# Optimization experiments

Measured on AMD Instinct MI355X. Metric: run time of the kernel, lower is better.

## Reference

```python
import jax, jax.numpy as jnp
import numpy as np

B, T = 128, 512
V, E, U, K = 50000, 100, 128, 32


def _lstm(x, Wk, Wr, b):
    # x: [B, T, D] -> [B, T, U], Keras LSTM gate order i,f,g,o
    Bd = x.shape[0]
    Ud = Wr.shape[0]
    xs = jnp.swapaxes(x, 0, 1)  # [T, B, D]

    def step(carry, xt):
        h, c = carry
        z = xt @ Wk + h @ Wr + b
        i, f, g, o = jnp.split(z, 4, axis=-1)
        c = jax.nn.sigmoid(f) * c + jax.nn.sigmoid(i) * jnp.tanh(g)
        h = jax.nn.sigmoid(o) * jnp.tanh(c)
        return (h, c), h

    init = (jnp.zeros((Bd, Ud), x.dtype), jnp.zeros((Bd, Ud), x.dtype))
    _, hs = jax.lax.scan(step, init, xs)
    return jnp.swapaxes(hs, 0, 1)


def _crf_logZ(em, trans):
    # em: [B, T, K] emissions; trans: [K, K]. Forward algorithm log-partition.
    alpha0 = em[:, 0]  # [B, K]
    es = jnp.swapaxes(em[:, 1:], 0, 1)  # [T-1, B, K]

    def step(alpha, et):
        # alpha[b, i] + trans[i, j] -> logsumexp over i, plus emission
        alpha = jax.nn.logsumexp(alpha[:, :, None] + trans[None], axis=1) + et
        return alpha, None

    alphaT, _ = jax.lax.scan(step, alpha0, es)
    return jax.nn.logsumexp(alphaT, axis=-1)  # [B]


def setup_inputs() -> dict:
    key = jax.random.key(0)
    ks = jax.random.split(key, 11)
    s = 0.1
    return {
        "tokens": jax.random.randint(ks[0], (B, T), 0, V, dtype=jnp.int32),
        "emb": jax.random.normal(ks[1], (V, E), jnp.float32) * s,
        "Wk_f": jax.random.normal(ks[2], (E, 4 * U), jnp.float32) * s,
        "Wr_f": jax.random.normal(ks[3], (U, 4 * U), jnp.float32) * s,
        "b_f": jnp.zeros((4 * U,), jnp.float32),
        "Wk_b": jax.random.normal(ks[4], (E, 4 * U), jnp.float32) * s,
        "Wr_b": jax.random.normal(ks[5], (U, 4 * U), jnp.float32) * s,
        "b_b": jnp.zeros((4 * U,), jnp.float32),
        "crf_kernel": jax.random.normal(ks[6], (2 * U, K), jnp.float32) * s,
        "crf_bias": jnp.zeros((K,), jnp.float32),
        "trans": jax.random.normal(ks[7], (K, K), jnp.float32) * s,
    }


def reference(tokens, emb, Wk_f, Wr_f, b_f, Wk_b, Wr_b, b_b, crf_kernel, crf_bias, trans):
    x = emb[tokens]  # [B, T, E]
    h_f = _lstm(x, Wk_f, Wr_f, b_f)
    h_b = _lstm(x[:, ::-1], Wk_b, Wr_b, b_b)[:, ::-1]
    h = jnp.concatenate([h_f, h_b], axis=-1)  # [B, T, 2U] (dropout = identity at inference)
    em = h @ crf_kernel + crf_bias  # [B, T, K] CRF emission potentials
    return _crf_logZ(em, trans)  # [B] log-partition via CRF forward DP
```

## Files before the change

kernel.cpp:

```cpp
#include <hip/hip_runtime.h>
#include <hip/hip_bf16.h>

#define B_  128
#define T_  512
#define V_  50000
#define VP  50016
#define E_  100
#define U_  128
#define K_  32
#define G4  512
#define KP  128
#define GRP 8

typedef _Float16 h2_t __attribute__((ext_vector_type(2)));
typedef _Float16 f16x8 __attribute__((ext_vector_type(8)));
typedef __fp16   h2raw_t __attribute__((ext_vector_type(2)));
typedef short    bf16x8 __attribute__((ext_vector_type(8)));
typedef float    f32x4  __attribute__((ext_vector_type(4)));

__device__ __forceinline__ h2_t pk2(float a, float b) {
    h2raw_t r = __builtin_amdgcn_cvt_pkrtz(a, b);
    union { h2raw_t r; h2_t h; } u; u.r = r; return u.h;
}
__device__ __forceinline__ int h2_as_int(h2_t v) { union { h2_t h; int i; } u; u.h = v; return u.i; }

#if __has_builtin(__builtin_amdgcn_rcpf)
__device__ __forceinline__ float rcp_f(float x) { return __builtin_amdgcn_rcpf(x); }
#else
__device__ __forceinline__ float rcp_f(float x) { return 1.f / x; }
#endif

__device__ __forceinline__ unsigned short bf16_bits(float v) {
    __hip_bfloat16 b = __float2bfloat16(v);
    union { __hip_bfloat16 b; unsigned short s; } u; u.b = b; return u.s;
}

__global__ __launch_bounds__(128) void pack_b_kernel(
    const float* __restrict__ Wk_f, const float* __restrict__ Wk_b,
    __hip_bfloat16* __restrict__ Bb)
{
    const int n = blockIdx.x;
    const int k = threadIdx.x;
    float v = 0.f;
    if (k < E_) v = (n < 512) ? Wk_f[k * 512 + n] : Wk_b[k * 512 + (n - 512)];
    Bb[n * KP + k] = __float2bfloat16(v);
}

__global__ __launch_bounds__(256, 2) void proj_mfma_kernel(
    const float* __restrict__ emb,
    const __hip_bfloat16* __restrict__ Bb,
    const float* __restrict__ b_f, const float* __restrict__ b_b,
    __hip_bfloat16* __restrict__ proj)
{
    const int r0   = blockIdx.x * 32;
    const int tid  = threadIdx.x;
    const int wv   = tid >> 6;
    const int lane = tid & 63;
    const int quad = lane >> 4;
    const int l16  = lane & 15;

    __shared__ __align__(16) float C_lds[32][268];
    unsigned short* A_st = (unsigned short*)&C_lds[0][0];

    for (int idx = tid; idx < 32 * 64; idx += 256) {
        int r = idx >> 6, kk = idx & 63;
        int vr = r0 + r; if (vr >= V_) vr = V_ - 1;
        unsigned int w = 0;
        if (kk < 50) {
            float2 v = *(const float2*)(emb + (long long)vr * E_ + 2 * kk);
            w = ((unsigned int)bf16_bits(v.y) << 16) | bf16_bits(v.x);
        }
        *(unsigned int*)&A_st[r * 136 + 2 * kk] = w;
    }
    __syncthreads();

    bf16x8 af[2][4];
    #pragma unroll
    for (int mt = 0; mt < 2; ++mt)
        #pragma unroll
        for (int kc = 0; kc < 4; ++kc)
            af[mt][kc] = *(const bf16x8*)&A_st[(mt * 16 + l16) * 136 +
                                               kc * 32 + quad * 8];
    __syncthreads();

    const unsigned short* Bu = (const unsigned short*)Bb;

    for (int ng = 0; ng < 4; ++ng) {
        const int n0 = ng * 256;

        bf16x8 bfr[4][4];
        #pragma unroll
        for (int nt = 0; nt < 4; ++nt)
            #pragma unroll
            for (int kc = 0; kc < 4; ++kc)
                bfr[nt][kc] = *(const bf16x8*)(Bu +
                    (n0 + wv * 64 + nt * 16 + l16) * KP + kc * 32 + quad * 8);

        f32x4 acc[2][4];
        #pragma unroll
        for (int mt = 0; mt < 2; ++mt)
            #pragma unroll
            for (int nt = 0; nt < 4; ++nt)
                acc[mt][nt] = (f32x4){0.f, 0.f, 0.f, 0.f};

        #pragma unroll
        for (int mt = 0; mt < 2; ++mt)
            #pragma unroll
            for (int nt = 0; nt < 4; ++nt)
                #pragma unroll
                for (int kc = 0; kc < 4; ++kc)
                    acc[mt][nt] = __builtin_amdgcn_mfma_f32_16x16x32_bf16(
                        af[mt][kc], bfr[nt][kc], acc[mt][nt], 0, 0, 0);

        #pragma unroll
        for (int mt = 0; mt < 2; ++mt)
            #pragma unroll
            for (int nt = 0; nt < 4; ++nt)
                #pragma unroll
                for (int v = 0; v < 4; ++v)
                    C_lds[mt * 16 + quad * 4 + v][wv * 64 + nt * 16 + l16] =
                        acc[mt][nt][v];
        __syncthreads();

        const float* bias = (n0 < 512) ? b_f : b_b;
        const int nbase = n0 & 511;
        for (int idx = tid; idx < 32 * 128; idx += 256) {
            int r = idx >> 7, cc = (idx & 127) * 2;
            float v0 = C_lds[r][cc]     + bias[nbase + cc];
            float v1 = C_lds[r][cc + 1] + bias[nbase + cc + 1];
            unsigned int w = ((unsigned int)bf16_bits(v1) << 16) | bf16_bits(v0);
            *(unsigned int*)(proj + (long long)(r0 + r) * 1024 + n0 + cc) = w;
        }
        __syncthreads();
    }
}

__device__ __forceinline__ float sigmoid_f(float x) {
    return rcp_f(1.f + __expf(-x));
}
__device__ __forceinline__ float tanh_f(float x) {
    return 1.f - 2.f * rcp_f(__expf(2.f * x) + 1.f);
}

__global__ __launch_bounds__(512, 1) void lstm_kernel(
    const __hip_bfloat16* __restrict__ proj,
    const int* __restrict__ tokens,
    const float* __restrict__ Wr_f, const float* __restrict__ Wr_b,
    __hip_bfloat16* __restrict__ h_buf)
{
    const int bid  = blockIdx.x;
    const int dir  = bid >> 7;
    const int b    = bid & 127;
    const int tid  = threadIdx.x;
    const int w    = tid >> 6;
    const int lane = tid & 63;
    const int quad = lane >> 4;
    const int l16  = lane & 15;

    const float* Wr = dir ? Wr_b : Wr_f;

    union uf16 { f16x8 v; h2_t p[4]; uint4 u; };
    f16x8 wb[4][4];
    #pragma unroll
    for (int tt = 0; tt < 4; ++tt) {
        const int col = 64 * w + 16 * tt + l16;
        #pragma unroll
        for (int kc = 0; kc < 4; ++kc) {
            const int k0 = kc * 32 + quad * 8;
            uf16 u;
            #pragma unroll
            for (int jj = 0; jj < 4; ++jj)
                u.p[jj] = pk2(Wr[(k0 + 2 * jj)     * G4 + col],
                              Wr[(k0 + 2 * jj + 1) * G4 + col]);
            wb[tt][kc] = u.v;
        }
    }

    __shared__ __align__(16) unsigned int hpl[64];
    __shared__ float zl[G4];
    if (tid < 64) hpl[tid] = 0;
    float c = 0.f;
    __syncthreads();

    const int tbase = b * T_;
    const long long rowbase = (long long)b * T_;
    const __hip_bfloat16* pr = proj + dir * 512 + tid;

    int tok_cur[GRP], tok_nxt[GRP];
    #pragma unroll
    for (int d = 0; d < GRP; ++d) {
        int t0 = dir ? (T_ - 1 - d) : d;
        tok_cur[d] = tokens[tbase + t0];
        int t1 = dir ? (T_ - 1 - (GRP + d)) : (GRP + d);
        tok_nxt[d] = tokens[tbase + t1];
    }

    float xk_cur[GRP][4];
    #pragma unroll
    for (int d = 0; d < GRP; ++d)
        #pragma unroll
        for (int g = 0; g < 4; ++g)
            xk_cur[d][g] = (tid < U_)
                ? __bfloat162float(pr[(long long)tok_cur[d] * 1024 + g * 128])
                : 0.f;

    unsigned int hpack[GRP];
    #pragma unroll
    for (int d = 0; d < GRP; ++d) hpack[d] = 0;

    for (int g = 0; g < T_ / GRP; ++g) {
        float xk_nxt[GRP][4];
        #pragma unroll
        for (int d = 0; d < GRP; ++d)
            #pragma unroll
            for (int gg = 0; gg < 4; ++gg) xk_nxt[d][gg] = 0.f;
        if (tid < U_ && g + 1 < T_ / GRP) {
            #pragma unroll
            for (int d = 0; d < GRP; ++d)
                #pragma unroll
                for (int gg = 0; gg < 4; ++gg)
                    xk_nxt[d][gg] = __bfloat162float(
                        pr[(long long)tok_nxt[d] * 1024 + gg * 128]);
        }
        int tok_n2[GRP];
        #pragma unroll
        for (int d = 0; d < GRP; ++d) tok_n2[d] = 0;
        if (g + 2 < T_ / GRP) {
            #pragma unroll
            for (int d = 0; d < GRP; ++d) {
                int s = (g + 2) * GRP + d;
                int t = dir ? (T_ - 1 - s) : s;
                tok_n2[d] = tokens[tbase + t];
            }
        }

        #pragma unroll
        for (int d = 0; d < GRP; ++d) {
            uf16 afr[4];
            #pragma unroll
            for (int kc = 0; kc < 4; ++kc)
                afr[kc].u = *(const uint4*)&hpl[kc * 16 + quad * 4];

            f32x4 acc[4];
            #pragma unroll
            for (int tt = 0; tt < 4; ++tt)
                acc[tt] = (f32x4){0.f, 0.f, 0.f, 0.f};
            #pragma unroll
            for (int tt = 0; tt < 4; ++tt)
                #pragma unroll
                for (int kc = 0; kc < 4; ++kc)
                    acc[tt] = __builtin_amdgcn_mfma_f32_16x16x32_f16(
                        afr[kc].v, wb[tt][kc], acc[tt], 0, 0, 0);

            float zv = (quad == 0) ? acc[0][0]
                     : (quad == 1) ? acc[1][0]
                     : (quad == 2) ? acc[2][0] : acc[3][0];
            zl[64 * w + lane] = zv;
            __syncthreads();

            if (tid < U_) {
                float zi = zl[tid]           + xk_cur[d][0];
                float zf = zl[U_ + tid]      + xk_cur[d][1];
                float zg = zl[2 * U_ + tid]  + xk_cur[d][2];
                float zo = zl[3 * U_ + tid]  + xk_cur[d][3];
                c = sigmoid_f(zf) * c + sigmoid_f(zi) * tanh_f(zg);
                float h = sigmoid_f(zo) * tanh_f(c);
                float hn = __shfl_down(h, 1, 64);
                if (!(tid & 1)) {
                    hpl[tid >> 1] = (unsigned int)h2_as_int(pk2(h, hn));
                    hpack[d] = ((unsigned int)bf16_bits(hn) << 16) | bf16_bits(h);
                }
            }
            __syncthreads();
        }

        if (tid < U_ && !(tid & 1)) {
            #pragma unroll
            for (int d = 0; d < GRP; ++d) {
                int s = g * GRP + d;
                int t = dir ? (T_ - 1 - s) : s;
                *(unsigned int*)(h_buf + (rowbase + t) * 256 + dir * U_ + tid) =
                    hpack[d];
            }
        }

        #pragma unroll
        for (int d = 0; d < GRP; ++d) {
            #pragma unroll
            for (int gg = 0; gg < 4; ++gg) xk_cur[d][gg] = xk_nxt[d][gg];
            tok_nxt[d] = tok_n2[d];
        }
    }
}

__global__ __launch_bounds__(256) void em_kernel(
    const __hip_bfloat16* __restrict__ h_buf,
    const float* __restrict__ ck, const float* __restrict__ cb,
    float* __restrict__ em)
{
    const int tid  = threadIdx.x;
    const int part = tid >> 5;
    const int k    = tid & 31;

    float ckr[32];
    #pragma unroll
    for (int i = 0; i < 32; ++i)
        ckr[i] = ck[(part * 32 + i) * K_ + k];
    const float cbk = cb[k];

    __shared__ float h_l[8][256];
    __shared__ float part_l[8][8][K_];

    const int r0 = blockIdx.x * 64;

    for (int round = 0; round < 8; ++round) {
        const int rbase = r0 + round * 8;
        #pragma unroll
        for (int j = 0; j < 8; ++j)
            h_l[j][tid] = __bfloat162float(h_buf[(long long)(rbase + j) * 256 + tid]);
        __syncthreads();

        #pragma unroll
        for (int j = 0; j < 8; ++j) {
            float pp = 0.f;
            #pragma unroll
            for (int i = 0; i < 32; ++i)
                pp = fmaf(h_l[j][part * 32 + i], ckr[i], pp);
            part_l[j][part][k] = pp;
        }
        __syncthreads();

        {
            int j2 = tid >> 5;
            float e = cbk;
            #pragma unroll
            for (int pq = 0; pq < 8; ++pq) e += part_l[j2][pq][k];
            em[(long long)(rbase + j2) * K_ + k] = e;
        }
        __syncthreads();
    }
}

#define PF_ 8
__global__ __launch_bounds__(64) void crf_kernel(
    const float* __restrict__ em,
    const float* __restrict__ trans,
    float* __restrict__ out)
{
    const int b    = blockIdx.x;
    const int lane = threadIdx.x;
    const int k    = lane & 31;
    const int half = lane >> 5;

    float etr[16];
    #pragma unroll
    for (int i = 0; i < 16; ++i)
        etr[i] = __expf(trans[(half * 16 + i) * K_ + k]);

    const float* em_b = em + (long long)b * T_ * K_;

    float ep[PF_];
    #pragma unroll
    for (int d = 0; d < PF_; ++d)
        ep[d] = em_b[d * K_ + k];

    float w = 0.f;
    float L = 0.f;
    for (int tb = 0; tb < T_; tb += PF_) {
        float en[PF_];
        if (tb + PF_ < T_) {
            #pragma unroll
            for (int d = 0; d < PF_; ++d)
                en[d] = em_b[(tb + PF_ + d) * K_ + k];
        } else {
            #pragma unroll
            for (int d = 0; d < PF_; ++d) en[d] = 0.f;
        }

        float eem[PF_];
        #pragma unroll
        for (int d = 0; d < PF_; ++d) eem[d] = __expf(ep[d]);

        #pragma unroll
        for (int d = 0; d < PF_; ++d) {
            if (tb + d == 0) {
                w = eem[d];
            } else {
                float acc = 0.f;
                #pragma unroll
                for (int i = 0; i < 16; ++i) {
                    float wv = __shfl(w, half * 16 + i, 64);
                    acc = fmaf(wv, etr[i], acc);
                }
                acc += __shfl_xor(acc, 32, 64);
                w = acc * eem[d];
            }
        }

        {
            float w0 = __shfl(w, 0, 64);
            w *= rcp_f(w0);
            L += __logf(w0);
        }

        #pragma unroll
        for (int d = 0; d < PF_; ++d) ep[d] = en[d];
    }

    float s = w;
    #pragma unroll
    for (int d = 1; d < 32; d <<= 1)
        s += __shfl_xor(s, d, 64);
    if (lane == 0) out[b] = L + __logf(s);
}

extern "C" void kernel_launch(void* const* d_in, const int* in_sizes, int n_in,
                              void* d_out, int out_size, void* d_ws, size_t ws_size,
                              hipStream_t stream)
{
    const int*   tokens = (const int*)  d_in[0];
    const float* emb    = (const float*)d_in[1];
    const float* Wk_f   = (const float*)d_in[2];
    const float* Wr_f   = (const float*)d_in[3];
    const float* b_f    = (const float*)d_in[4];
    const float* Wk_b   = (const float*)d_in[5];
    const float* Wr_b   = (const float*)d_in[6];
    const float* b_b    = (const float*)d_in[7];
    const float* ck     = (const float*)d_in[8];
    const float* cb     = (const float*)d_in[9];
    const float* trans  = (const float*)d_in[10];
    float* out = (float*)d_out;

    const long long ROWS = (long long)B_ * T_;
    __hip_bfloat16* proj  = (__hip_bfloat16*)d_ws;
    __hip_bfloat16* h_buf = proj + (long long)VP * 1024;
    float* em = (float*)(h_buf + ROWS * 256);
    __hip_bfloat16* Bb = (__hip_bfloat16*)(em + ROWS * K_);

    hipLaunchKernelGGL(pack_b_kernel, dim3(1024), dim3(128), 0, stream,
                       Wk_f, Wk_b, Bb);
    hipLaunchKernelGGL(proj_mfma_kernel, dim3(VP / 32), dim3(256), 0, stream,
                       emb, Bb, b_f, b_b, proj);
    hipLaunchKernelGGL(lstm_kernel, dim3(256), dim3(512), 0, stream,
                       proj, tokens, Wr_f, Wr_b, h_buf);
    hipLaunchKernelGGL(em_kernel, dim3((int)(ROWS / 64)), dim3(256), 0, stream,
                       h_buf, ck, cb, em);
    hipLaunchKernelGGL(crf_kernel, dim3(B_), dim3(64), 0, stream,
                       em, trans, out);
}
```

Baseline: 625.5 us.

## Remap LSTM recurrent MFMA columns so each wave owns whole units, drop z exchange

Reassigns recurrent weight columns so each wave computes all four gates for 16 hidden units, letting gate nonlinearities run directly from MFMA accumulators instead of routing z through shared memory. The h state is double-buffered in LDS as fp16, which cuts per-step barriers from two to one. Launch bounds are also raised to allow two blocks per CU. The trade-off is that all waves now redundantly compute activations across the four quads and load projections, and the higher occupancy target may cap registers and cause spills of the large unrolled state.

```diff
diff --git a/kernel.cpp b/kernel.cpp
--- a/kernel.cpp
+++ b/kernel.cpp
@@ -22,7 +22,6 @@
     h2raw_t r = __builtin_amdgcn_cvt_pkrtz(a, b);
     union { h2raw_t r; h2_t h; } u; u.r = r; return u.h;
 }
-__device__ __forceinline__ int h2_as_int(h2_t v) { union { h2_t h; int i; } u; u.h = v; return u.i; }
 
 #if __has_builtin(__builtin_amdgcn_rcpf)
 __device__ __forceinline__ float rcp_f(float x) { return __builtin_amdgcn_rcpf(x); }
@@ -142,7 +141,7 @@
     return 1.f - 2.f * rcp_f(__expf(2.f * x) + 1.f);
 }
 
-__global__ __launch_bounds__(512, 1) void lstm_kernel(
+__global__ __launch_bounds__(512, 2) void lstm_kernel(
     const __hip_bfloat16* __restrict__ proj,
     const int* __restrict__ tokens,
     const float* __restrict__ Wr_f, const float* __restrict__ Wr_b,
@@ -156,14 +155,15 @@
     const int lane = tid & 63;
     const int quad = lane >> 4;
     const int l16  = lane & 15;
+    const int unit = 16 * w + l16;
 
     const float* Wr = dir ? Wr_b : Wr_f;
 
-    union uf16 { f16x8 v; h2_t p[4]; uint4 u; };
+    union uf16 { f16x8 v; h2_t p[4]; };
     f16x8 wb[4][4];
     #pragma unroll
-    for (int tt = 0; tt < 4; ++tt) {
-        const int col = 64 * w + 16 * tt + l16;
+    for (int gq = 0; gq < 4; ++gq) {
+        const int col = gq * 128 + unit;
         #pragma unroll
         for (int kc = 0; kc < 4; ++kc) {
             const int k0 = kc * 32 + quad * 8;
@@ -172,19 +172,18 @@
             for (int jj = 0; jj < 4; ++jj)
                 u.p[jj] = pk2(Wr[(k0 + 2 * jj)     * G4 + col],
                               Wr[(k0 + 2 * jj + 1) * G4 + col]);
-            wb[tt][kc] = u.v;
-        }
-    }
-
-    __shared__ __align__(16) unsigned int hpl[64];
-    __shared__ float zl[G4];
-    if (tid < 64) hpl[tid] = 0;
+            wb[gq][kc] = u.v;
+        }
+    }
+
+    __shared__ __align__(16) _Float16 hpl[2][128];
+    if (tid < 128) hpl[0][tid] = (_Float16)0.f;
     float c = 0.f;
     __syncthreads();
 
     const int tbase = b * T_;
     const long long rowbase = (long long)b * T_;
-    const __hip_bfloat16* pr = proj + dir * 512 + tid;
+    const __hip_bfloat16* pr = proj + dir * 512 + unit;
 
     int tok_cur[GRP], tok_nxt[GRP];
     #pragma unroll
@@ -200,9 +199,8 @@
     for (int d = 0; d < GRP; ++d)
         #pragma unroll
         for (int g = 0; g < 4; ++g)
-            xk_cur[d][g] = (tid < U_)
-                ? __bfloat162float(pr[(long long)tok_cur[d] * 1024 + g * 128])
-                : 0.f;
+            xk_cur[d][g] = __bfloat162float(
+                pr[(long long)tok_cur[d] * 1024 + g * 128]);
 
     unsigned int hpack[GRP];
     #pragma unroll
@@ -214,7 +212,7 @@
         for (int d = 0; d < GRP; ++d)
             #pragma unroll
             for (int gg = 0; gg < 4; ++gg) xk_nxt[d][gg] = 0.f;
-        if (tid < U_ && g + 1 < T_ / GRP) {
+        if (g + 1 < T_ / GRP) {
             #pragma unroll
             for (int d = 0; d < GRP; ++d)
                 #pragma unroll
@@ -236,50 +234,44 @@
 
         #pragma unroll
         for (int d = 0; d < GRP; ++d) {
-            uf16 afr[4];
+            f16x8 a[4];
             #pragma unroll
             for (int kc = 0; kc < 4; ++kc)
-                afr[kc].u = *(const uint4*)&hpl[kc * 16 + quad * 4];
+                a[kc] = *(const f16x8*)&hpl[d & 1][kc * 32 + quad * 8];
 
             f32x4 acc[4];
             #pragma unroll
-            for (int tt = 0; tt < 4; ++tt)
-                acc[tt] = (f32x4){0.f, 0.f, 0.f, 0.f};
-            #pragma unroll
-            for (int tt = 0; tt < 4; ++tt)
+            for (int gq = 0; gq < 4; ++gq)
+                acc[gq] = (f32x4){0.f, 0.f, 0.f, 0.f};
+            #pragma unroll
+            for (int gq = 0; gq < 4; ++gq)
                 #pragma unroll
                 for (int kc = 0; kc < 4; ++kc)
-                    acc[tt] = __builtin_amdgcn_mfma_f32_16x16x32_f16(
-                        afr[kc].v, wb[tt][kc], acc[tt], 0, 0, 0);
-
-            float zv = (quad == 0) ? acc[0][0]
-                     : (quad == 1) ? acc[1][0]
-                     : (quad == 2) ? acc[2][0] : acc[3][0];
-            zl[64 * w + lane] = zv;
+                    acc[gq] = __builtin_amdgcn_mfma_f32_16x16x32_f16(
+                        a[kc], wb[gq][kc], acc[gq], 0, 0, 0);
+
+            float zi = acc[0][0] + xk_cur[d][0];
+            float zf = acc[1][0] + xk_cur[d][1];
+            float zg = acc[2][0] + xk_cur[d][2];
+            float zo = acc[3][0] + xk_cur[d][3];
+            c = sigmoid_f(zf) * c + sigmoid_f(zi) * tanh_f(zg);
+            float h = sigmoid_f(zo) * tanh_f(c);
+
+            if (quad == 0) hpl[(d + 1) & 1][unit] = (_Float16)h;
+
+            float hn = __shfl_down(h, 1, 64);
+            if (quad == 0 && !(l16 & 1))
+                hpack[d] = ((unsigned int)bf16_bits(hn) << 16) | bf16_bits(h);
+
             __syncthreads();
-
-            if (tid < U_) {
-                float zi = zl[tid]           + xk_cur[d][0];
-                float zf = zl[U_ + tid]      + xk_cur[d][1];
-                float zg = zl[2 * U_ + tid]  + xk_cur[d][2];
-                float zo = zl[3 * U_ + tid]  + xk_cur[d][3];
-                c = sigmoid_f(zf) * c + sigmoid_f(zi) * tanh_f(zg);
-                float h = sigmoid_f(zo) * tanh_f(c);
-                float hn = __shfl_down(h, 1, 64);
-                if (!(tid & 1)) {
-                    hpl[tid >> 1] = (unsigned int)h2_as_int(pk2(h, hn));
-                    hpack[d] = ((unsigned int)bf16_bits(hn) << 16) | bf16_bits(h);
-                }
-            }
-            __syncthreads();
-        }
-
-        if (tid < U_ && !(tid & 1)) {
+        }
+
+        if (quad == 0 && !(l16 & 1)) {
             #pragma unroll
             for (int d = 0; d < GRP; ++d) {
                 int s = g * GRP + d;
                 int t = dir ? (T_ - 1 - s) : s;
-                *(unsigned int*)(h_buf + (rowbase + t) * 256 + dir * U_ + tid) =
+                *(unsigned int*)(h_buf + (rowbase + t) * 256 + dir * U_ + unit) =
                     hpack[d];
             }
         }
```

New measurement: 598.1 us. 4.4% less time.
